# Kernel optimization log

Measured on AMD Instinct MI355X. Metric: run time of the kernel, lower is better.

The kernel has to match this reference:

```python
import jax, jax.numpy as jnp
import numpy as np

N_HEADS = 8
LN_EPS = 1e-5
NEG = -1e9


def _layernorm(x, g, b):
    mu = jnp.mean(x, axis=-1, keepdims=True)
    var = jnp.var(x, axis=-1, keepdims=True)
    return (x - mu) * jax.lax.rsqrt(var + LN_EPS) * g + b


def setup_inputs() -> dict:
    key = jax.random.key(0)
    ks = jax.random.split(key, 16)
    B, T, D, W, L, A = 8, 256, 512, 32, 4, 6
    s = 0.02
    return {
        "feats": jax.random.normal(ks[0], (B, T, D), jnp.float32),
        "pos_embed": jax.random.normal(ks[1], (1, W, D), jnp.float32) * s,
        "Wqkv": jax.random.normal(ks[2], (L, 3 * D, D), jnp.float32) * s,
        "bqkv": jnp.zeros((L, 3 * D), jnp.float32),
        "Wo": jax.random.normal(ks[3], (L, D, D), jnp.float32) * s,
        "bo": jnp.zeros((L, D), jnp.float32),
        "ln1_g": jnp.ones((L, D), jnp.float32),
        "ln1_b": jnp.zeros((L, D), jnp.float32),
        "W1": jax.random.normal(ks[4], (L, 4 * D, D), jnp.float32) * s,
        "b1": jnp.zeros((L, 4 * D), jnp.float32),
        "W2": jax.random.normal(ks[5], (L, D, 4 * D), jnp.float32) * s,
        "b2": jnp.zeros((L, D), jnp.float32),
        "ln2_g": jnp.ones((L, D), jnp.float32),
        "ln2_b": jnp.zeros((L, D), jnp.float32),
        "Wp": jax.random.normal(ks[6], (A, D), jnp.float32) * s,
        "bp": jnp.zeros((A,), jnp.float32),
        "Wv": jax.random.normal(ks[7], (1, D), jnp.float32) * s,
        "bv": jnp.zeros((1,), jnp.float32),
    }


def reference(feats, pos_embed, Wqkv, bqkv, Wo, bo, ln1_g, ln1_b,
              W1, b1, W2, b2, ln2_g, ln2_b, Wp, bp, Wv, bv):
    B, T, D = feats.shape
    W = pos_embed.shape[1]
    L = Wqkv.shape[0]
    H = N_HEADS
    dh = D // H

    # Sliding windows for every timestep t: window slot w holds frame
    # max(t+1-W+w, 0)  (left-pad short prefixes by repeating frame 0).
    idx = jnp.maximum(jnp.arange(T)[:, None] + 1 - W + jnp.arange(W)[None, :], 0)  # (T,W)
    x = feats[:, idx, :].reshape(B * T, W, D) + pos_embed  # (B*T, W, D)

    causal = jnp.tril(jnp.ones((W, W), bool))  # additive -inf upper-tri mask

    for i in range(L):
        qkv = x @ Wqkv[i].T + bqkv[i]                     # (N,W,3D)
        q, k, v = jnp.split(qkv, 3, axis=-1)
        q = q.reshape(-1, W, H, dh).transpose(0, 2, 1, 3)
        k = k.reshape(-1, W, H, dh).transpose(0, 2, 1, 3)
        v = v.reshape(-1, W, H, dh).transpose(0, 2, 1, 3)
        scores = jnp.einsum('nhqd,nhkd->nhqk', q, k) / jnp.sqrt(jnp.float32(dh))
        scores = jnp.where(causal, scores, NEG)
        attn = jax.nn.softmax(scores, axis=-1)
        ctx = jnp.einsum('nhqk,nhkd->nhqd', attn, v)
        ctx = ctx.transpose(0, 2, 1, 3).reshape(-1, W, D)
        x = _layernorm(x + ctx @ Wo[i].T + bo[i], ln1_g[i], ln1_b[i])
        ff = jax.nn.relu(x @ W1[i].T + b1[i]) @ W2[i].T + b2[i]
        x = _layernorm(x + ff, ln2_g[i], ln2_b[i])

    token = x[:, -1, :].reshape(B, T, D)
    logits = token @ Wp.T + bp          # (B,T,A)
    values = (token @ Wv.T + bv)[..., 0]  # (B,T)
    return logits, values
```

## Files before the change

### kernel.cpp

```cpp
#include <hip/hip_runtime.h>
#include <hip/hip_bf16.h>
#include <cstdint>
#include <cstddef>

#define B_    8
#define T_    256
#define D_    512
#define W_    32
#define L_    4
#define A_    6
#define H_    8
#define DH_   64
#define NWIN  (B_*T_)
#define NTOK  (NWIN*W_)
#define FROWS 2176
#define SMALL (NWIN*D_)

typedef __hip_bfloat16 bf16;
using bf16x8 = __attribute__((ext_vector_type(8))) short;
using f32x4  = __attribute__((ext_vector_type(4))) float;
using f32x16 = __attribute__((ext_vector_type(16))) float;

#define XB_BYTES  ((size_t)NTOK * D_ * 2)
#define WQ_ELEMS  ((size_t)L_ * 3*D_*D_)
#define WO_ELEMS  ((size_t)L_ * D_*D_)
#define W1_ELEMS  ((size_t)L_ * 4*D_*D_)
#define W2_ELEMS  ((size_t)L_ * 4*D_*D_)
#define WB_BYTES  ((WQ_ELEMS + WO_ELEMS + W1_ELEMS + W2_ELEMS) * 2)
#define FB_ELEMS  ((size_t)FROWS * D_)
#define QF_ELEMS  ((size_t)FROWS * 3*D_)
#define PPB_ELEMS ((size_t)W_ * 3*D_)
#define SCR_BYTES ((size_t)NTOK * 2560 * 2)
#define TOTAL_BYTES (XB_BYTES + WB_BYTES + (FB_ELEMS + QF_ELEMS)*2 + PPB_ELEMS*4 + SCR_BYTES)

static char* g_fallback = nullptr;
__attribute__((constructor)) static void alloc_fallback() {
    (void)hipMalloc((void**)&g_fallback, TOTAL_BYTES);
}

typedef __attribute__((address_space(3))) uint8_t* as3p;
typedef const __attribute__((address_space(1))) uint8_t* as1p;
__device__ __forceinline__ void gload_lds16(const void* g, void* l) {
    __builtin_amdgcn_global_load_lds((as1p)(const uint8_t*)g,
                                     (as3p)(uint32_t)(uintptr_t)l, 16, 0, 0);
}

__device__ __forceinline__ float bf2f(short s) {
    return __uint_as_float(((uint32_t)(uint16_t)s) << 16);
}
__device__ __forceinline__ short f2bf(float f) {
    return (short)__bfloat16_as_ushort(__float2bfloat16(f));
}

__global__ __launch_bounds__(256) void cvt_kernel(
    const float* __restrict__ w, bf16* __restrict__ o, int n4)
{
    int i = blockIdx.x * 256 + threadIdx.x;
    if (i >= n4) return;
    float4 f = ((const float4*)w)[i];
    bf16* d = o + (size_t)i * 4;
    d[0] = __float2bfloat16(f.x);
    d[1] = __float2bfloat16(f.y);
    d[2] = __float2bfloat16(f.z);
    d[3] = __float2bfloat16(f.w);
}

__global__ __launch_bounds__(256) void build_x_kernel(
    const float* __restrict__ feats,
    const float* __restrict__ pos,
    bf16* __restrict__ xb)
{
    int gid   = blockIdx.x * 256 + threadIdx.x;
    int token = gid >> 7;
    int c4    = (gid & 127) * 4;
    int w     = token & (W_-1);
    int n     = token >> 5;
    int t     = n & (T_-1);
    int b     = n >> 8;
    int frame = t + w - (W_-1); if (frame < 0) frame = 0;
    const float4 f = *(const float4*)(feats + ((size_t)(b*T_ + frame)*D_ + c4));
    const float4 p = *(const float4*)(pos   + ((size_t)w*D_ + c4));
    bf16* d = xb + (size_t)token*D_ + c4;
    d[0] = __float2bfloat16(f.x + p.x);
    d[1] = __float2bfloat16(f.y + p.y);
    d[2] = __float2bfloat16(f.z + p.z);
    d[3] = __float2bfloat16(f.w + p.w);
}

__global__ __launch_bounds__(256) void build_fb_kernel(
    const float* __restrict__ feats,
    const float* __restrict__ pos,
    bf16* __restrict__ fb)
{
    int gid = blockIdx.x * 256 + threadIdx.x;
    int row = gid >> 7;
    int c4  = (gid & 127) * 4;
    bf16* d = fb + (size_t)row * D_ + c4;
    float4 f;
    if (row < 2048)      f = *(const float4*)(feats + (size_t)row * D_ + c4);
    else if (row < 2080) f = *(const float4*)(pos + (size_t)(row - 2048) * D_ + c4);
    else                 f = make_float4(0.f, 0.f, 0.f, 0.f);
    d[0] = __float2bfloat16(f.x);
    d[1] = __float2bfloat16(f.y);
    d[2] = __float2bfloat16(f.z);
    d[3] = __float2bfloat16(f.w);
}

__global__ __launch_bounds__(256) void build_ppb_kernel(
    const bf16* __restrict__ qf,
    const float* __restrict__ bq,
    float* __restrict__ ppb)
{
    int gid = blockIdx.x * 256 + threadIdx.x;
    int w = gid / (3*D_), c = gid % (3*D_);
    ppb[gid] = bf2f(*(const short*)(qf + (size_t)(2048 + w) * (3*D_) + c)) + bq[c];
}

__global__ __launch_bounds__(256) void slice31_kernel(
    const bf16* __restrict__ xb, bf16* __restrict__ xg)
{
    int gid = blockIdx.x * 256 + threadIdx.x;
    int n = gid >> 6, c0 = (gid & 63) * 8;
    *(bf16x8*)(xg + (size_t)n*D_ + c0) =
        *(const bf16x8*)(xb + (size_t)(n*W_ + (W_-1))*D_ + c0);
}

template<bool RELU, bool BIAS, bool REMAP>
__global__ __launch_bounds__(256) void gemm_bf16(
    const bf16* __restrict__ A,
    const bf16* __restrict__ Bt,
    const float* __restrict__ bias,
    bf16* __restrict__ Cb,
    int M, int N, int K)
{
    __shared__ bf16 As[128*32];
    __shared__ bf16 Bs[128*32];

    const int tid  = threadIdx.x;
    const int lane = tid & 63;
    const int wv   = tid >> 6;

    const int gridN = N >> 7;
    const int bid   = blockIdx.x;
    int m0, n0;
    if (REMAP) {
        const int q_ = bid >> 3;
        n0 = (q_ % gridN) << 7;
        m0 = (((q_ / gridN) * 8) + (bid & 7)) << 7;
    } else {
        n0 = (bid % gridN) << 7;
        m0 = (bid / gridN) << 7;
    }

    const int wm = (wv >> 1) * 64;
    const int wn = (wv & 1) * 64;

    f32x16 acc[2][2] = {};

    const int   srow  = wv*16 + (lane >> 2);
    const int   skoff = (lane & 3) * 8;
    const bf16* ga0 = A  + (size_t)(m0 + srow)      * K + skoff;
    const bf16* ga1 = A  + (size_t)(m0 + 64 + srow) * K + skoff;
    const bf16* gb0 = Bt + (size_t)(n0 + srow)      * K + skoff;
    const bf16* gb1 = Bt + (size_t)(n0 + 64 + srow) * K + skoff;
    char* lAs = (char*)As;
    char* lBs = (char*)Bs;
    const int l0 = wv*1024 + lane*16;

    const int r32  = lane & 31;
    const int ksel = (lane >> 5) * 16;

    for (int k0 = 0; k0 < K; k0 += 32) {
        gload_lds16(ga0 + k0, lAs + l0);
        gload_lds16(ga1 + k0, lAs + l0 + 4096);
        gload_lds16(gb0 + k0, lBs + l0);
        gload_lds16(gb1 + k0, lBs + l0 + 4096);
        __syncthreads();

        bf16x8 av[2][2], bv[2][2];
#pragma unroll
        for (int i = 0; i < 2; ++i)
#pragma unroll
            for (int h = 0; h < 2; ++h) {
                av[i][h] = *(const bf16x8*)(lAs + (wm + i*32 + r32)*64 + h*32 + ksel);
                bv[i][h] = *(const bf16x8*)(lBs + (wn + i*32 + r32)*64 + h*32 + ksel);
            }
#pragma unroll
        for (int i = 0; i < 2; ++i)
#pragma unroll
            for (int j = 0; j < 2; ++j) {
                acc[i][j] = __builtin_amdgcn_mfma_f32_32x32x16_bf16(
                    av[i][0], bv[j][0], acc[i][j], 0, 0, 0);
                acc[i][j] = __builtin_amdgcn_mfma_f32_32x32x16_bf16(
                    av[i][1], bv[j][1], acc[i][j], 0, 0, 0);
            }
        __syncthreads();
    }

    const int rbase = (lane >> 5) * 4;
#pragma unroll
    for (int i = 0; i < 2; ++i) {
#pragma unroll
        for (int j = 0; j < 2; ++j) {
            const int ncol = n0 + wn + j*32 + r32;
            const float bv_ = BIAS ? bias[ncol] : 0.f;
#pragma unroll
            for (int reg = 0; reg < 16; ++reg) {
                const int mrow = m0 + wm + i*32 + (reg & 3) + 8*(reg >> 2) + rbase;
                float v = acc[i][j][reg] + bv_;
                if (RELU) v = fmaxf(v, 0.f);
                Cb[(size_t)mrow * N + ncol] = __float2bfloat16(v);
            }
        }
    }
}

template<bool RELU, bool BIAS>
__global__ __launch_bounds__(512, 2) void gemm256(
    const bf16* __restrict__ A,
    const bf16* __restrict__ Bt,
    const float* __restrict__ bias,
    bf16* __restrict__ Cb,
    int M, int N, int K)
{
    (void)M;
    __shared__ bf16 As[2][256*64];
    __shared__ bf16 Bs[2][256*64];

    const int tid  = threadIdx.x;
    const int lane = tid & 63;
    const int wv   = tid >> 6;
    const int wm   = wv >> 2;
    const int wn   = wv & 3;
    const int L    = lane & 15;
    const int qd   = lane >> 4;

    const int gridN = N >> 8;
    const int W8  = gridN << 3;
    const int bid = blockIdx.x;
    const int q_  = bid / W8;
    const int r_  = bid % W8;
    const int n0  = (r_ >> 3) << 8;
    const int m0  = ((q_ << 3) + (r_ & 7)) << 8;

    const int srow = tid >> 3;
    const int scol = ((tid & 7) ^ (srow & 7)) * 8;
    const bf16* gA = A  + (size_t)(m0 + srow) * K + scol;
    const bf16* gB = Bt + (size_t)(n0 + srow) * K + scol;
    const size_t rstep = (size_t)64 * K;
    bf16* lA = &As[0][0] + tid * 8;
    bf16* lB = &Bs[0][0] + tid * 8;

    const int physk0 = ((qd)     ^ (L & 7)) * 8;
    const int physk1 = ((4 + qd) ^ (L & 7)) * 8;
    const int aoff = (wm*128 + L) * 64;
    const int boff = (wn*64  + L) * 64;

    f32x4 acc[8][4] = {};
    bf16x8 av0[4][2], av1[4][2], bv0[2][2], bv1[2][2];

#define STAGE_A2(b, kt) do { \
    const bf16* s_ = gA + (size_t)(kt) * 64; \
    bf16* d_ = lA + (b) * 16384; \
    gload_lds16(s_,            d_); \
    gload_lds16(s_ +   rstep,  d_ + 4096); \
    gload_lds16(s_ + 2*rstep,  d_ + 8192); \
    gload_lds16(s_ + 3*rstep,  d_ + 12288); } while (0)

#define STAGE_B2(b, kt) do { \
    const bf16* s_ = gB + (size_t)(kt) * 64; \
    bf16* d_ = lB + (b) * 16384; \
    gload_lds16(s_,            d_); \
    gload_lds16(s_ +   rstep,  d_ + 4096); \
    gload_lds16(s_ + 2*rstep,  d_ + 8192); \
    gload_lds16(s_ + 3*rstep,  d_ + 12288); } while (0)

#define LDA_(dst, b, qm) do { \
    const bf16* pa_ = &As[b][aoff + (qm)*4096]; \
    _Pragma("unroll") \
    for (int mr_ = 0; mr_ < 4; ++mr_) { \
        dst[mr_][0] = *(const bf16x8*)(pa_ + mr_*1024 + physk0); \
        dst[mr_][1] = *(const bf16x8*)(pa_ + mr_*1024 + physk1); } } while (0)

#define LDB_(dst, b, qn) do { \
    const bf16* pb_ = &Bs[b][boff + (qn)*2048]; \
    _Pragma("unroll") \
    for (int nr_ = 0; nr_ < 2; ++nr_) { \
        dst[nr_][0] = *(const bf16x8*)(pb_ + nr_*1024 + physk0); \
        dst[nr_][1] = *(const bf16x8*)(pb_ + nr_*1024 + physk1); } } while (0)

#define MMA_(qm, qn, av, bv) do { \
    _Pragma("unroll") \
    for (int mr_ = 0; mr_ < 4; ++mr_) \
    _Pragma("unroll") \
    for (int nr_ = 0; nr_ < 2; ++nr_) { \
        f32x4 c_ = acc[(qm)*4+mr_][(qn)*2+nr_]; \
        c_ = __builtin_amdgcn_mfma_f32_16x16x32_bf16(av[mr_][0], bv[nr_][0], c_, 0, 0, 0); \
        c_ = __builtin_amdgcn_mfma_f32_16x16x32_bf16(av[mr_][1], bv[nr_][1], c_, 0, 0, 0); \
        acc[(qm)*4+mr_][(qn)*2+nr_] = c_; } } while (0)

#define BAR_ __builtin_amdgcn_s_barrier()
#define LGKM0_ do { asm volatile("s_waitcnt lgkmcnt(0)" ::: "memory"); \
                    __builtin_amdgcn_sched_barrier(0); } while (0)

#define TILE_(b, kt2) do { \
     \
    LDA_(av0, b, 0); LDB_(bv0, b, 0); \
    BAR_; LGKM0_; \
    __builtin_amdgcn_s_setprio(1); MMA_(0, 0, av0, bv0); __builtin_amdgcn_s_setprio(0); \
    BAR_; \
     \
    LDB_(bv1, b, 1); \
    BAR_; LGKM0_; \
    __builtin_amdgcn_s_setprio(1); MMA_(0, 1, av0, bv1); __builtin_amdgcn_s_setprio(0); \
    BAR_; \
     \
    LDA_(av1, b, 1); \
    STAGE_B2(b, kt2); \
    BAR_; LGKM0_; \
    __builtin_amdgcn_s_setprio(1); MMA_(1, 1, av1, bv1); __builtin_amdgcn_s_setprio(0); \
    BAR_; \
     \
    STAGE_A2(b, kt2); \
    __builtin_amdgcn_s_setprio(1); MMA_(1, 0, av1, bv0); __builtin_amdgcn_s_setprio(0); \
    asm volatile("s_waitcnt vmcnt(8)" ::: "memory"); \
    BAR_; } while (0)

    const int nkt = K >> 6;

    STAGE_B2(0, 0); STAGE_A2(0, 0);
    STAGE_B2(1, 1); STAGE_A2(1, 1);
    asm volatile("s_waitcnt vmcnt(8)" ::: "memory");
    BAR_;

    for (int u = 0; u < nkt; u += 2) {
        int k2 = u + 2; if (k2 >= nkt) k2 -= nkt;
        int k3 = u + 3; if (k3 >= nkt) k3 -= nkt;
        TILE_(0, k2);
        TILE_(1, k3);
    }

    asm volatile("s_waitcnt vmcnt(0)" ::: "memory");

#pragma unroll
    for (int mr = 0; mr < 8; ++mr) {
        const int row = m0 + wm*128 + mr*16 + qd*4;
#pragma unroll
        for (int nr = 0; nr < 4; ++nr) {
            const int col = n0 + wn*64 + nr*16 + L;
            const float bb = BIAS ? bias[col] : 0.f;
            bf16* cp = Cb + (size_t)row * N + col;
#pragma unroll
            for (int rg = 0; rg < 4; ++rg) {
                float v = acc[mr][nr][rg] + bb;
                if (RELU) v = fmaxf(v, 0.f);
                cp[(size_t)rg * N] = __float2bfloat16(v);
            }
        }
    }

#undef STAGE_A2
#undef STAGE_B2
#undef LDA_
#undef LDB_
#undef MMA_
#undef BAR_
#undef LGKM0_
#undef TILE_
}

__global__ __launch_bounds__(256) void lnres_kernel(
    const bf16* __restrict__ y,
    const bf16* __restrict__ xin,
    bf16* __restrict__ xout,
    const float* __restrict__ g,
    const float* __restrict__ b,
    int xin_stride)
{
    const int wave  = threadIdx.x >> 6;
    const int lane  = threadIdx.x & 63;
    const int token = blockIdx.x * 4 + wave;
    const int c0    = lane * 8;

    const bf16* yr = y    + (size_t)token * D_ + c0;
    const bf16* xr = xin  + (size_t)token * xin_stride + c0;
    bf16*       xo = xout + (size_t)token * D_ + c0;

    bf16x8 ty = *(const bf16x8*)yr;
    bf16x8 tx = *(const bf16x8*)xr;

    float v[8];
    float s1 = 0.f, s2 = 0.f;
#pragma unroll
    for (int j = 0; j < 8; ++j) {
        v[j] = bf2f(ty[j]) + bf2f(tx[j]);
        s1 += v[j]; s2 += v[j]*v[j];
    }
#pragma unroll
    for (int mask = 1; mask < 64; mask <<= 1) {
        s1 += __shfl_xor(s1, mask);
        s2 += __shfl_xor(s2, mask);
    }
    const float mu = s1 * (1.f / D_);
    float var = s2 * (1.f / D_) - mu * mu;
    if (var < 0.f) var = 0.f;
    const float rs = rsqrtf(var + 1e-5f);

    const float4 g0 = *(const float4*)(g + c0);
    const float4 g1 = *(const float4*)(g + c0 + 4);
    const float4 b0 = *(const float4*)(b + c0);
    const float4 b1 = *(const float4*)(b + c0 + 4);
    const float gg[8] = {g0.x,g0.y,g0.z,g0.w,g1.x,g1.y,g1.z,g1.w};
    const float bb[8] = {b0.x,b0.y,b0.z,b0.w,b1.x,b1.y,b1.z,b1.w};

    bf16x8 o;
#pragma unroll
    for (int j = 0; j < 8; ++j) {
        float t = (v[j] - mu) * rs * gg[j] + bb[j];
        o[j] = f2bf(t);
    }
    *(bf16x8*)xo = o;
}

__global__ __launch_bounds__(256) void attn_mfma(
    const bf16* __restrict__ qkv,
    bf16* __restrict__ ctx)
{
    __shared__ short Pb[4][32*32];

    const int tid  = threadIdx.x;
    const int lane = tid & 63;
    const int wv   = tid >> 6;
    const int pair = blockIdx.x * 4 + wv;
    const int win  = pair >> 3;
    const int h    = pair & 7;

    const int quad = lane >> 4;
    const int col  = lane & 15;

    const bf16* base = qkv + (size_t)win * W_ * (3*D_) + h * DH_;

    bf16x8 bvv[4];
    {
        const short* vbase = (const short*)(base + 2*D_);
#pragma unroll
        for (int ntd = 0; ntd < 4; ++ntd)
#pragma unroll
            for (int jj = 0; jj < 8; ++jj)
                bvv[ntd][jj] = vbase[(size_t)(quad*8 + jj) * (3*D_) + ntd*16 + col];
    }

    bf16x8 aq[2][2], bk[2][2];
#pragma unroll
    for (int mt = 0; mt < 2; ++mt)
#pragma unroll
        for (int kq = 0; kq < 2; ++kq)
            aq[mt][kq] = *(const bf16x8*)(base + (size_t)(mt*16 + col) * (3*D_)
                                          + kq*32 + quad*8);
#pragma unroll
    for (int nt = 0; nt < 2; ++nt)
#pragma unroll
        for (int kq = 0; kq < 2; ++kq)
            bk[nt][kq] = *(const bf16x8*)(base + D_ + (size_t)(nt*16 + col) * (3*D_)
                                          + kq*32 + quad*8);

    f32x4 S[2][2] = {};
#pragma unroll
    for (int mt = 0; mt < 2; ++mt)
#pragma unroll
        for (int nt = 0; nt < 2; ++nt) {
            S[mt][nt] = __builtin_amdgcn_mfma_f32_16x16x32_bf16(
                aq[mt][0], bk[nt][0], S[mt][nt], 0, 0, 0);
            S[mt][nt] = __builtin_amdgcn_mfma_f32_16x16x32_bf16(
                aq[mt][1], bk[nt][1], S[mt][nt], 0, 0, 0);
        }

    short* P = Pb[wv];
#pragma unroll
    for (int mt = 0; mt < 2; ++mt) {
#pragma unroll
        for (int reg = 0; reg < 4; ++reg) {
            const int row = mt*16 + quad*4 + reg;
            float v0 = (col      <= row) ? S[mt][0][reg] * 0.125f : -1e30f;
            float v1 = (16 + col <= row) ? S[mt][1][reg] * 0.125f : -1e30f;
            float mx = fmaxf(v0, v1);
#pragma unroll
            for (int m = 1; m < 16; m <<= 1) mx = fmaxf(mx, __shfl_xor(mx, m));
            float e0 = __expf(v0 - mx);
            float e1 = __expf(v1 - mx);
            float sm = e0 + e1;
#pragma unroll
            for (int m = 1; m < 16; m <<= 1) sm += __shfl_xor(sm, m);
            float inv = 1.f / sm;
            P[row*32 + col]      = f2bf(e0 * inv);
            P[row*32 + 16 + col] = f2bf(e1 * inv);
        }
    }

    bf16* cb = ctx + (size_t)win * W_ * D_ + h * DH_;
#pragma unroll
    for (int mt = 0; mt < 2; ++mt) {
        bf16x8 ap = *(const bf16x8*)(P + (mt*16 + col)*32 + quad*8);
#pragma unroll
        for (int ntd = 0; ntd < 4; ++ntd) {
            f32x4 O = {};
            O = __builtin_amdgcn_mfma_f32_16x16x32_bf16(ap, bvv[ntd], O, 0, 0, 0);
#pragma unroll
            for (int reg = 0; reg < 4; ++reg) {
                const int row = mt*16 + quad*4 + reg;
                cb[(size_t)row * D_ + ntd*16 + col] = __float2bfloat16(O[reg]);
            }
        }
    }
}

__global__ __launch_bounds__(256) void attn_mfma0(
    const bf16* __restrict__ qf,
    const float* __restrict__ ppb,
    bf16* __restrict__ ctx)
{
    __shared__ short Pb[4][32*32];

    const int tid  = threadIdx.x;
    const int lane = tid & 63;
    const int wv   = tid >> 6;
    const int pair = blockIdx.x * 4 + wv;
    const int win  = pair >> 3;
    const int h    = pair & 7;

    const int quad = lane >> 4;
    const int col  = lane & 15;
    const int bb_  = win >> 8;
    const int tt_  = win & (T_-1);

#define FR_(w) ((size_t)(bb_*T_ + ((tt_ + (w) - (W_-1)) > 0 ? (tt_ + (w) - (W_-1)) : 0)) * (3*D_))

    bf16x8 bvv[4];
#pragma unroll
    for (int ntd = 0; ntd < 4; ++ntd)
#pragma unroll
        for (int jj = 0; jj < 8; ++jj) {
            const int w2 = quad*8 + jj;
            const int c  = 2*D_ + h*DH_ + ntd*16 + col;
            bvv[ntd][jj] = f2bf(bf2f(*(const short*)(qf + FR_(w2) + c))
                                + ppb[w2*(3*D_) + c]);
        }

    bf16x8 aq[2][2], bk[2][2];
#pragma unroll
    for (int mt = 0; mt < 2; ++mt)
#pragma unroll
        for (int kq = 0; kq < 2; ++kq) {
            const int w  = mt*16 + col;
            const size_t fro = FR_(w);
            const int cq = h*DH_ + kq*32 + quad*8;
            const bf16x8 a = *(const bf16x8*)(qf + fro + cq);
            const bf16x8 k = *(const bf16x8*)(qf + fro + D_ + cq);
            const float* pq = ppb + w*(3*D_) + cq;
            const float* pk = pq + D_;
#pragma unroll
            for (int j = 0; j < 8; ++j) {
                aq[mt][kq][j] = f2bf(bf2f(a[j]) + pq[j]);
                bk[mt][kq][j] = f2bf(bf2f(k[j]) + pk[j]);
            }
        }
#undef FR_

    f32x4 S[2][2] = {};
#pragma unroll
    for (int mt = 0; mt < 2; ++mt)
#pragma unroll
        for (int nt = 0; nt < 2; ++nt) {
            S[mt][nt] = __builtin_amdgcn_mfma_f32_16x16x32_bf16(
                aq[mt][0], bk[nt][0], S[mt][nt], 0, 0, 0);
            S[mt][nt] = __builtin_amdgcn_mfma_f32_16x16x32_bf16(
                aq[mt][1], bk[nt][1], S[mt][nt], 0, 0, 0);
        }

    short* P = Pb[wv];
#pragma unroll
    for (int mt = 0; mt < 2; ++mt) {
#pragma unroll
        for (int reg = 0; reg < 4; ++reg) {
            const int row = mt*16 + quad*4 + reg;
            float v0 = (col      <= row) ? S[mt][0][reg] * 0.125f : -1e30f;
            float v1 = (16 + col <= row) ? S[mt][1][reg] * 0.125f : -1e30f;
            float mx = fmaxf(v0, v1);
#pragma unroll
            for (int m = 1; m < 16; m <<= 1) mx = fmaxf(mx, __shfl_xor(mx, m));
            float e0 = __expf(v0 - mx);
            float e1 = __expf(v1 - mx);
            float sm = e0 + e1;
#pragma unroll
            for (int m = 1; m < 16; m <<= 1) sm += __shfl_xor(sm, m);
            float inv = 1.f / sm;
            P[row*32 + col]      = f2bf(e0 * inv);
            P[row*32 + 16 + col] = f2bf(e1 * inv);
        }
    }

    bf16* cb = ctx + (size_t)win * W_ * D_ + h * DH_;
#pragma unroll
    for (int mt = 0; mt < 2; ++mt) {
        bf16x8 ap = *(const bf16x8*)(P + (mt*16 + col)*32 + quad*8);
#pragma unroll
        for (int ntd = 0; ntd < 4; ++ntd) {
            f32x4 O = {};
            O = __builtin_amdgcn_mfma_f32_16x16x32_bf16(ap, bvv[ntd], O, 0, 0, 0);
#pragma unroll
            for (int reg = 0; reg < 4; ++reg) {
                const int row = mt*16 + quad*4 + reg;
                cb[(size_t)row * D_ + ntd*16 + col] = __float2bfloat16(O[reg]);
            }
        }
    }
}

__global__ __launch_bounds__(256) void attn_last2(
    const bf16* __restrict__ kv,
    const bf16* __restrict__ q31,
    bf16* __restrict__ ctxl)
{
    __shared__ float Ps[4][32];

    const int wv   = threadIdx.x >> 6;
    const int lane = threadIdx.x & 63;
    const int pair = blockIdx.x * 4 + wv;
    const int win  = pair >> 3;
    const int h    = pair & 7;

    const bf16* kb   = kv + (size_t)win * W_ * 1024 + h * DH_;
    const short* qrow = (const short*)(q31 + (size_t)win * D_ + h * DH_);

    const int k    = lane & 31;
    const int half = lane >> 5;
    const short* krow = (const short*)(kb + (size_t)k * 1024 + half*32);

    float s = 0.f;
    const bf16x8* q8 = (const bf16x8*)(qrow + half*32);
    const bf16x8* k8 = (const bf16x8*)krow;
#pragma unroll
    for (int c = 0; c < 4; ++c) {
        bf16x8 qa = q8[c], kb_ = k8[c];
#pragma unroll
        for (int j = 0; j < 8; ++j) s += bf2f(qa[j]) * bf2f(kb_[j]);
    }
    s += __shfl_xor(s, 32);
    s *= 0.125f;

    float mx = s;
#pragma unroll
    for (int m = 1; m < 32; m <<= 1) mx = fmaxf(mx, __shfl_xor(mx, m));
    float e = __expf(s - mx);
    float sum = e;
#pragma unroll
    for (int m = 1; m < 32; m <<= 1) sum += __shfl_xor(sum, m);
    if (half == 0) Ps[wv][k] = e / sum;
    __syncthreads();

    const short* vb = (const short*)(kb + 512);
    float o = 0.f;
#pragma unroll
    for (int kk = 0; kk < 32; ++kk)
        o += Ps[wv][kk] * bf2f(vb[(size_t)kk * 1024 + lane]);

    ctxl[(size_t)win * D_ + h * DH_ + lane] = __float2bfloat16(o);
}

__global__ __launch_bounds__(64) void head_kernel(
    const bf16* __restrict__ xq,
    const float* __restrict__ Wp, const float* __restrict__ bp,
    const float* __restrict__ Wv, const float* __restrict__ bv,
    float* __restrict__ out)
{
    const int n    = blockIdx.x;
    const int lane = threadIdx.x;
    const bf16* row = xq + (size_t)n * D_;
    float t[8];
#pragma unroll
    for (int j = 0; j < 8; ++j) t[j] = bf2f(*(const short*)(row + lane + j*64));

    for (int a = 0; a < A_ + 1; ++a) {
        const float* w = (a < A_) ? (Wp + (size_t)a * D_) : Wv;
        float d = 0.f;
#pragma unroll
        for (int j = 0; j < 8; ++j) d += t[j] * w[lane + j*64];
#pragma unroll
        for (int off = 32; off > 0; off >>= 1) d += __shfl_down(d, off);
        if (lane == 0) {
            if (a < A_) out[(size_t)n*A_ + a] = d + bp[a];
            else        out[(size_t)NWIN*A_ + n] = d + bv[0];
        }
    }
}

extern "C" void kernel_launch(void* const* d_in, const int* in_sizes, int n_in,
                              void* d_out, int out_size, void* d_ws, size_t ws_size,
                              hipStream_t stream) {
    const float* feats = (const float*)d_in[0];
    const float* pos   = (const float*)d_in[1];
    const float* Wqkv  = (const float*)d_in[2];
    const float* bqkv  = (const float*)d_in[3];
    const float* Wo    = (const float*)d_in[4];
    const float* bo    = (const float*)d_in[5];
    const float* ln1g  = (const float*)d_in[6];
    const float* ln1b  = (const float*)d_in[7];
    const float* W1    = (const float*)d_in[8];
    const float* b1    = (const float*)d_in[9];
    const float* W2    = (const float*)d_in[10];
    const float* b2    = (const float*)d_in[11];
    const float* ln2g  = (const float*)d_in[12];
    const float* ln2b  = (const float*)d_in[13];
    const float* Wp    = (const float*)d_in[14];
    const float* bp    = (const float*)d_in[15];
    const float* Wv    = (const float*)d_in[16];
    const float* bv    = (const float*)d_in[17];
    float* out = (float*)d_out;

    char* basep = (ws_size >= TOTAL_BYTES) ? (char*)d_ws : g_fallback;

    bf16*  xb   = (bf16*)basep;
    bf16*  wq_b = (bf16*)(basep + XB_BYTES);
    bf16*  wo_b = wq_b + WQ_ELEMS;
    bf16*  w1_b = wo_b + WO_ELEMS;
    bf16*  w2_b = w1_b + W1_ELEMS;
    bf16*  fb   = w2_b + W2_ELEMS;
    bf16*  qf   = fb + FB_ELEMS;
    float* ppb  = (float*)(qf + QF_ELEMS);
    bf16*  scr  = (bf16*)(ppb + PPB_ELEMS);
    bf16*  qkv_s = scr;
    bf16*  kv_s  = scr;
    bf16*  ctx_s = scr + (size_t)NTOK * (3*D_);
    bf16*  h_s   = scr;
    bf16*  y_s   = scr + (size_t)NTOK * 2048;
    bf16*  ctxl = ctx_s;
    bf16*  ysm  = ctx_s + (size_t)SMALL;
    bf16*  hsm  = ctx_s + (size_t)2*SMALL;
    bf16*  xq   = ctx_s + (size_t)6*SMALL;
    bf16*  xg   = ctx_s + (size_t)8*SMALL;
    bf16*  q31  = ctx_s + (size_t)9*SMALL;

    cvt_kernel<<<(WQ_ELEMS/4 + 255)/256, 256, 0, stream>>>(Wqkv, wq_b, WQ_ELEMS/4);
    cvt_kernel<<<(WO_ELEMS/4 + 255)/256, 256, 0, stream>>>(Wo,   wo_b, WO_ELEMS/4);
    cvt_kernel<<<(W1_ELEMS/4 + 255)/256, 256, 0, stream>>>(W1,   w1_b, W1_ELEMS/4);
    cvt_kernel<<<(W2_ELEMS/4 + 255)/256, 256, 0, stream>>>(W2,   w2_b, W2_ELEMS/4);

    build_x_kernel<<<NTOK * (D_/4) / 256, 256, 0, stream>>>(feats, pos, xb);
    build_fb_kernel<<<FROWS * (D_/4) / 256, 256, 0, stream>>>(feats, pos, fb);

    const int GM2 = NTOK / 256;

    for (int i = 0; i < L_; ++i) {
        const bf16*  wq_i = wq_b + (size_t)i * 3*D_*D_;
        const float* bq_i = bqkv + (size_t)i * 3*D_;
        const bf16*  wo_i = wo_b + (size_t)i * D_*D_;
        const float* bo_i = bo   + (size_t)i * D_;
        const bf16*  w1_i = w1_b + (size_t)i * 4*D_*D_;
        const float* b1_i = b1   + (size_t)i * 4*D_;
        const bf16*  w2_i = w2_b + (size_t)i * 4*D_*D_;
        const float* b2_i = b2   + (size_t)i * D_;

        if (i == 0) {
            gemm_bf16<false,false,false><<<(FROWS/128) * (3*D_/128), 256, 0, stream>>>(
                fb, wq_i, nullptr, qf, FROWS, 3*D_, D_);
            build_ppb_kernel<<<W_*(3*D_)/256, 256, 0, stream>>>(qf, bq_i, ppb);
            attn_mfma0<<<NWIN * H_ / 4, 256, 0, stream>>>(qf, ppb, ctx_s);
        } else if (i < L_-1) {
            gemm256<false,true><<<GM2 * (3*D_/256), 512, 0, stream>>>(
                xb, wq_i, bq_i, qkv_s, NTOK, 3*D_, D_);
            attn_mfma<<<NWIN * H_ / 4, 256, 0, stream>>>(qkv_s, ctx_s);
        }

        if (i < L_-1) {
            gemm256<false,true><<<GM2 * (D_/256), 512, 0, stream>>>(
                ctx_s, wo_i, bo_i, y_s, NTOK, D_, D_);
            lnres_kernel<<<NTOK/4, 256, 0, stream>>>(
                y_s, xb, xb, ln1g + (size_t)i*D_, ln1b + (size_t)i*D_, D_);
            gemm256<true,true><<<GM2 * (4*D_/256), 512, 0, stream>>>(
                xb, w1_i, b1_i, h_s, NTOK, 4*D_, D_);
            gemm256<false,true><<<GM2 * (D_/256), 512, 0, stream>>>(
                h_s, w2_i, b2_i, y_s, NTOK, D_, 4*D_);
            lnres_kernel<<<NTOK/4, 256, 0, stream>>>(
                y_s, xb, xb, ln2g + (size_t)i*D_, ln2b + (size_t)i*D_, D_);
        } else {
            gemm256<false,true><<<GM2 * (1024/256), 512, 0, stream>>>(
                xb, wq_i + (size_t)D_*D_, bq_i + D_, kv_s, NTOK, 2*D_, D_);
            slice31_kernel<<<NWIN*64/256, 256, 0, stream>>>(xb, xg);
            gemm_bf16<false,true,false><<<(NWIN/128) * (D_/128), 256, 0, stream>>>(
                xg, wq_i, bq_i, q31, NWIN, D_, D_);
            attn_last2<<<NWIN * H_ / 4, 256, 0, stream>>>(kv_s, q31, ctxl);
            gemm_bf16<false,true,false><<<(NWIN/128) * (D_/128), 256, 0, stream>>>(
                ctxl, wo_i, bo_i, ysm, NWIN, D_, D_);
            lnres_kernel<<<NWIN/4, 256, 0, stream>>>(
                ysm, xg, xq,
                ln1g + (size_t)i*D_, ln1b + (size_t)i*D_, D_);
            gemm_bf16<true,true,false><<<(NWIN/128) * (4*D_/128), 256, 0, stream>>>(
                xq, w1_i, b1_i, hsm, NWIN, 4*D_, D_);
            gemm_bf16<false,true,false><<<(NWIN/128) * (D_/128), 256, 0, stream>>>(
                hsm, w2_i, b2_i, ysm, NWIN, D_, 4*D_);
            lnres_kernel<<<NWIN/4, 256, 0, stream>>>(
                ysm, xq, xq, ln2g + (size_t)i*D_, ln2b + (size_t)i*D_, D_);
        }
    }

    head_kernel<<<NWIN, 64, 0, stream>>>(xq, Wp, bp, Wv, bv, out);
}
```

Baseline: 2.056 ms.

## Fuse Wo and W2 GEMMs with residual add and LayerNorm

Measured after the change: 2.236 ms. 1.09x slower.

```diff
diff --git a/kernel.cpp b/kernel.cpp
--- a/kernel.cpp
+++ b/kernel.cpp
@@ -369,6 +369,157 @@
 #undef TILE_
 }
 
+__global__ __launch_bounds__(512, 2) void gemmln(
+    const bf16* __restrict__ A,
+    const bf16* __restrict__ Bt,
+    const float* __restrict__ bias,
+    bf16* __restrict__ xb,
+    const float* __restrict__ g,
+    const float* __restrict__ b,
+    int K)
+{
+    __shared__ bf16 As[3*128*32];
+    __shared__ bf16 Bs[3*512*32];
+
+    const int tid  = threadIdx.x;
+    const int lane = tid & 63;
+    const int wv   = tid >> 6;
+    const int wm   = wv >> 2;
+    const int wn   = wv & 3;
+    const int L    = lane & 15;
+    const int qd   = lane >> 4;
+
+    const int m0 = blockIdx.x << 7;
+
+    const int srow = tid >> 2;
+    const int slog = (tid & 3) ^ ((srow >> 1) & 3);
+    const bf16* gA = A  + (size_t)(m0 + srow) * K + slog * 8;
+    const bf16* gB = Bt + (size_t)srow * K + slog * 8;
+    const size_t rb = (size_t)128 * K;
+    bf16* lA = As + tid * 8;
+    bf16* lB = Bs + tid * 8;
+
+    const int kch  = (qd ^ ((L >> 1) & 3)) * 8;
+    const int aoff = (wm*64  + L) * 32 + kch;
+    const int boff = (wn*128 + L) * 32 + kch;
+
+    f32x4 acc[4][8] = {};
+
+#define STG_(buf, kt) do { \
+    gload_lds16(gA + (size_t)(kt) * 32, lA + (buf) * 4096); \
+    const bf16* s_ = gB + (size_t)(kt) * 32; \
+    bf16* d_ = lB + (buf) * 16384; \
+    gload_lds16(s_,         d_); \
+    gload_lds16(s_ +   rb,  d_ + 4096); \
+    gload_lds16(s_ + 2*rb,  d_ + 8192); \
+    gload_lds16(s_ + 3*rb,  d_ + 12288); } while (0)
+
+#define BAR_ __builtin_amdgcn_s_barrier()
+
+    const int nt = K >> 5;
+
+    STG_(0, 0);
+    STG_(1, 1);
+    asm volatile("s_waitcnt vmcnt(5)" ::: "memory");
+    BAR_;
+
+    int b0 = 0;
+    for (int t = 0; t < nt; ++t) {
+        const int tgt = (b0 + 2 >= 3) ? b0 - 1 : b0 + 2;
+        const int kt2 = (t + 2 < nt) ? t + 2 : t;
+        STG_(tgt, kt2);
+
+        bf16x8 av[4], bv[8];
+        const bf16* pa = As + b0*4096  + aoff;
+        const bf16* pb = Bs + b0*16384 + boff;
+#pragma unroll
+        for (int mr = 0; mr < 4; ++mr) av[mr] = *(const bf16x8*)(pa + mr*512);
+#pragma unroll
+        for (int nr = 0; nr < 8; ++nr) bv[nr] = *(const bf16x8*)(pb + nr*512);
+        asm volatile("s_waitcnt lgkmcnt(0)" ::: "memory");
+        __builtin_amdgcn_sched_barrier(0);
+        __builtin_amdgcn_s_setprio(1);
+#pragma unroll
+        for (int mr = 0; mr < 4; ++mr)
+#pragma unroll
+            for (int nr = 0; nr < 8; ++nr)
+                acc[mr][nr] = __builtin_amdgcn_mfma_f32_16x16x32_bf16(
+                    av[mr], bv[nr], acc[mr][nr], 0, 0, 0);
+        __builtin_amdgcn_s_setprio(0);
+        asm volatile("s_waitcnt vmcnt(5)" ::: "memory");
+        BAR_;
+        b0 = (b0 == 2) ? 0 : b0 + 1;
+    }
+
+    asm volatile("s_waitcnt vmcnt(0)" ::: "memory");
+    BAR_;
+
+    float* lnred = (float*)As;
+
+    float bias8[8], gg8[8], bb8[8];
+#pragma unroll
+    for (int nr = 0; nr < 8; ++nr) {
+        const int col = wn*128 + nr*16 + L;
+        bias8[nr] = bias[col];
+        gg8[nr]   = g[col];
+        bb8[nr]   = b[col];
+    }
+
+#pragma unroll
+    for (int mr = 0; mr < 4; ++mr) {
+#pragma unroll
+        for (int rg = 0; rg < 4; ++rg) {
+            const int row = wm*64 + mr*16 + qd*4 + rg;
+            const bf16* xr = xb + (size_t)(m0 + row) * D_ + wn*128 + L;
+            float ps = 0.f, pq = 0.f;
+#pragma unroll
+            for (int nr = 0; nr < 8; ++nr) {
+                float s = acc[mr][nr][rg] + bias8[nr]
+                        + bf2f(*(const short*)(xr + nr*16));
+                acc[mr][nr][rg] = s;
+                ps += s; pq += s*s;
+            }
+#pragma unroll
+            for (int m = 1; m < 16; m <<= 1) {
+                ps += __shfl_xor(ps, m);
+                pq += __shfl_xor(pq, m);
+            }
+            if (L == 0) {
+                lnred[(wn*128 + row)*2    ] = ps;
+                lnred[(wn*128 + row)*2 + 1] = pq;
+            }
+        }
+    }
+    BAR_;
+
+#pragma unroll
+    for (int mr = 0; mr < 4; ++mr) {
+#pragma unroll
+        for (int rg = 0; rg < 4; ++rg) {
+            const int row = wm*64 + mr*16 + qd*4 + rg;
+            float S = 0.f, Q = 0.f;
+#pragma unroll
+            for (int w4 = 0; w4 < 4; ++w4) {
+                S += lnred[(w4*128 + row)*2    ];
+                Q += lnred[(w4*128 + row)*2 + 1];
+            }
+            const float mu = S * (1.f / D_);
+            float var = Q * (1.f / D_) - mu * mu;
+            if (var < 0.f) var = 0.f;
+            const float rs = rsqrtf(var + 1e-5f);
+            bf16* xw = xb + (size_t)(m0 + row) * D_ + wn*128 + L;
+#pragma unroll
+            for (int nr = 0; nr < 8; ++nr) {
+                float o = (acc[mr][nr][rg] - mu) * rs * gg8[nr] + bb8[nr];
+                *(short*)(xw + nr*16) = f2bf(o);
+            }
+        }
+    }
+
+#undef STG_
+#undef BAR_
+}
+
 __global__ __launch_bounds__(256) void lnres_kernel(
     const bf16* __restrict__ y,
     const bf16* __restrict__ xin,
@@ -732,7 +883,6 @@
     bf16*  kv_s  = scr;
     bf16*  ctx_s = scr + (size_t)NTOK * (3*D_);
     bf16*  h_s   = scr;
-    bf16*  y_s   = scr + (size_t)NTOK * 2048;
     bf16*  ctxl = ctx_s;
     bf16*  ysm  = ctx_s + (size_t)SMALL;
     bf16*  hsm  = ctx_s + (size_t)2*SMALL;
@@ -749,6 +899,7 @@
     build_fb_kernel<<<FROWS * (D_/4) / 256, 256, 0, stream>>>(feats, pos, fb);
 
     const int GM2 = NTOK / 256;
+    const int GL  = NTOK / 128;
 
     for (int i = 0; i < L_; ++i) {
         const bf16*  wq_i = wq_b + (size_t)i * 3*D_*D_;
@@ -772,16 +923,14 @@
         }
 
         if (i < L_-1) {
-            gemm256<false,true><<<GM2 * (D_/256), 512, 0, stream>>>(
-                ctx_s, wo_i, bo_i, y_s, NTOK, D_, D_);
-            lnres_kernel<<<NTOK/4, 256, 0, stream>>>(
-                y_s, xb, xb, ln1g + (size_t)i*D_, ln1b + (size_t)i*D_, D_);
+            gemmln<<<GL, 512, 0, stream>>>(
+                ctx_s, wo_i, bo_i, xb,
+                ln1g + (size_t)i*D_, ln1b + (size_t)i*D_, D_);
             gemm256<true,true><<<GM2 * (4*D_/256), 512, 0, stream>>>(
                 xb, w1_i, b1_i, h_s, NTOK, 4*D_, D_);
-            gemm256<false,true><<<GM2 * (D_/256), 512, 0, stream>>>(
-                h_s, w2_i, b2_i, y_s, NTOK, D_, 4*D_);
-            lnres_kernel<<<NTOK/4, 256, 0, stream>>>(
-                y_s, xb, xb, ln2g + (size_t)i*D_, ln2b + (size_t)i*D_, D_);
+            gemmln<<<GL, 512, 0, stream>>>(
+                h_s, w2_i, b2_i, xb,
+                ln2g + (size_t)i*D_, ln2b + (size_t)i*D_, 4*D_);
         } else {
             gemm256<false,true><<<GM2 * (1024/256), 512, 0, stream>>>(
                 xb, wq_i + (size_t)D_*D_, bq_i + D_, kv_s, NTOK, 2*D_, D_);
```

## Use persistent multi-panel GEMM kernel for FFN layers with fixed grid

Applied to the files above, without the earlier changes.

Result: faster. 1.999 ms (-2.8%).

```diff
diff --git a/kernel.cpp b/kernel.cpp
--- a/kernel.cpp
+++ b/kernel.cpp
@@ -369,6 +369,165 @@
 #undef TILE_
 }
 
+template<bool RELU, int LOG2NKT, int NPAN>
+__global__ __launch_bounds__(512, 2) void gemm256m(
+    const bf16* __restrict__ A,
+    const bf16* __restrict__ Bt,
+    const float* __restrict__ bias,
+    bf16* __restrict__ Cb,
+    int N)
+{
+    constexpr int NKT = 1 << LOG2NKT;
+    constexpr int K   = NKT * 64;
+    constexpr int NT  = NPAN * NKT;
+
+    __shared__ bf16 As[2][256*64];
+    __shared__ bf16 Bs[2][256*64];
+
+    const int tid  = threadIdx.x;
+    const int lane = tid & 63;
+    const int wv   = tid >> 6;
+    const int wm   = wv >> 2;
+    const int wn   = wv & 3;
+    const int L    = lane & 15;
+    const int qd   = lane >> 4;
+
+    const int gridN = N >> 8;
+    const int SETS  = 256 / gridN;
+    const int bid   = blockIdx.x;
+    const int sI    = bid % SETS;
+    const int n0    = (bid / SETS) << 8;
+
+    const int srow = tid >> 3;
+    const int scol = ((tid & 7) ^ (srow & 7)) * 8;
+    const bf16* gA0 = A  + (size_t)srow * K + scol;
+    const bf16* gB  = Bt + (size_t)(n0 + srow) * K + scol;
+    const size_t rstep = (size_t)64 * K;
+    bf16* lA = &As[0][0] + tid * 8;
+    bf16* lB = &Bs[0][0] + tid * 8;
+
+    const int physk0 = ((qd)     ^ (L & 7)) * 8;
+    const int physk1 = ((4 + qd) ^ (L & 7)) * 8;
+    const int aoff = (wm*128 + L) * 64;
+    const int boff = (wn*64  + L) * 64;
+
+    f32x4 acc[8][4] = {};
+    bf16x8 av0[4][2], av1[4][2], bv0[2][2], bv1[2][2];
+
+#define MSTAGE_A(b, tau) do { \
+    const int p2_ = (tau) >> LOG2NKT, k2_ = (tau) & (NKT-1); \
+    const bf16* s_ = gA0 + ((size_t)(sI + SETS*p2_) << 8) * K + (size_t)k2_ * 64; \
+    bf16* d_ = lA + (b) * 16384; \
+    gload_lds16(s_,            d_); \
+    gload_lds16(s_ +   rstep,  d_ + 4096); \
+    gload_lds16(s_ + 2*rstep,  d_ + 8192); \
+    gload_lds16(s_ + 3*rstep,  d_ + 12288); } while (0)
+
+#define MSTAGE_B(b, tau) do { \
+    const bf16* s_ = gB + (size_t)((tau) & (NKT-1)) * 64; \
+    bf16* d_ = lB + (b) * 16384; \
+    gload_lds16(s_,            d_); \
+    gload_lds16(s_ +   rstep,  d_ + 4096); \
+    gload_lds16(s_ + 2*rstep,  d_ + 8192); \
+    gload_lds16(s_ + 3*rstep,  d_ + 12288); } while (0)
+
+#define MLDA(dst, b, qm) do { \
+    const bf16* pa_ = &As[b][aoff + (qm)*4096]; \
+    _Pragma("unroll") \
+    for (int mr_ = 0; mr_ < 4; ++mr_) { \
+        dst[mr_][0] = *(const bf16x8*)(pa_ + mr_*1024 + physk0); \
+        dst[mr_][1] = *(const bf16x8*)(pa_ + mr_*1024 + physk1); } } while (0)
+
+#define MLDB(dst, b, qn) do { \
+    const bf16* pb_ = &Bs[b][boff + (qn)*2048]; \
+    _Pragma("unroll") \
+    for (int nr_ = 0; nr_ < 2; ++nr_) { \
+        dst[nr_][0] = *(const bf16x8*)(pb_ + nr_*1024 + physk0); \
+        dst[nr_][1] = *(const bf16x8*)(pb_ + nr_*1024 + physk1); } } while (0)
+
+#define MMMA(qm, qn, av, bv) do { \
+    _Pragma("unroll") \
+    for (int mr_ = 0; mr_ < 4; ++mr_) \
+    _Pragma("unroll") \
+    for (int nr_ = 0; nr_ < 2; ++nr_) { \
+        f32x4 c_ = acc[(qm)*4+mr_][(qn)*2+nr_]; \
+        c_ = __builtin_amdgcn_mfma_f32_16x16x32_bf16(av[mr_][0], bv[nr_][0], c_, 0, 0, 0); \
+        c_ = __builtin_amdgcn_mfma_f32_16x16x32_bf16(av[mr_][1], bv[nr_][1], c_, 0, 0, 0); \
+        acc[(qm)*4+mr_][(qn)*2+nr_] = c_; } } while (0)
+
+#define MBAR __builtin_amdgcn_s_barrier()
+#define MLGKM0 do { asm volatile("s_waitcnt lgkmcnt(0)" ::: "memory"); \
+                    __builtin_amdgcn_sched_barrier(0); } while (0)
+
+#define MTILE(b, tau2) do { \
+     \
+    MLDA(av0, b, 0); MLDB(bv0, b, 0); \
+    MBAR; MLGKM0; \
+    __builtin_amdgcn_s_setprio(1); MMMA(0, 0, av0, bv0); __builtin_amdgcn_s_setprio(0); \
+    MBAR; \
+     \
+    MLDB(bv1, b, 1); \
+    MBAR; MLGKM0; \
+    __builtin_amdgcn_s_setprio(1); MMMA(0, 1, av0, bv1); __builtin_amdgcn_s_setprio(0); \
+    MBAR; \
+     \
+    MLDA(av1, b, 1); \
+    MSTAGE_B(b, tau2); \
+    MBAR; MLGKM0; \
+    __builtin_amdgcn_s_setprio(1); MMMA(1, 1, av1, bv1); __builtin_amdgcn_s_setprio(0); \
+    MBAR; \
+     \
+    MSTAGE_A(b, tau2); \
+    __builtin_amdgcn_s_setprio(1); MMMA(1, 0, av1, bv0); __builtin_amdgcn_s_setprio(0); \
+    asm volatile("s_waitcnt vmcnt(8)" ::: "memory"); \
+    MBAR; } while (0)
+
+    MSTAGE_B(0, 0); MSTAGE_A(0, 0);
+    MSTAGE_B(1, 1); MSTAGE_A(1, 1);
+    asm volatile("s_waitcnt vmcnt(8)" ::: "memory");
+    MBAR;
+
+    for (int u = 0; u < NT; u += 2) {
+        const int t2 = (u + 2 < NT) ? u + 2 : u;
+        const int t3 = (u + 3 < NT) ? u + 3 : u + 1;
+        MTILE(0, t2);
+        MTILE(1, t3);
+
+        if (((u + 1) & (NKT - 1)) == NKT - 1) {
+            const int panel = (u + 1) >> LOG2NKT;
+            const int mbase = (sI + SETS * panel) << 8;
+#pragma unroll
+            for (int mr = 0; mr < 8; ++mr) {
+                const int row = mbase + wm*128 + mr*16 + qd*4;
+#pragma unroll
+                for (int nr = 0; nr < 4; ++nr) {
+                    const int col = n0 + wn*64 + nr*16 + L;
+                    const float bb = bias[col];
+                    bf16* cp = Cb + (size_t)row * N + col;
+#pragma unroll
+                    for (int rg = 0; rg < 4; ++rg) {
+                        float v = acc[mr][nr][rg] + bb;
+                        if (RELU) v = fmaxf(v, 0.f);
+                        cp[(size_t)rg * N] = __float2bfloat16(v);
+                    }
+                    acc[mr][nr] = (f32x4){0.f, 0.f, 0.f, 0.f};
+                }
+            }
+        }
+    }
+
+    asm volatile("s_waitcnt vmcnt(0)" ::: "memory");
+
+#undef MSTAGE_A
+#undef MSTAGE_B
+#undef MLDA
+#undef MLDB
+#undef MMMA
+#undef MBAR
+#undef MLGKM0
+#undef MTILE
+}
+
 __global__ __launch_bounds__(256) void lnres_kernel(
     const bf16* __restrict__ y,
     const bf16* __restrict__ xin,
@@ -776,10 +935,10 @@
                 ctx_s, wo_i, bo_i, y_s, NTOK, D_, D_);
             lnres_kernel<<<NTOK/4, 256, 0, stream>>>(
                 y_s, xb, xb, ln1g + (size_t)i*D_, ln1b + (size_t)i*D_, D_);
-            gemm256<true,true><<<GM2 * (4*D_/256), 512, 0, stream>>>(
-                xb, w1_i, b1_i, h_s, NTOK, 4*D_, D_);
-            gemm256<false,true><<<GM2 * (D_/256), 512, 0, stream>>>(
-                h_s, w2_i, b2_i, y_s, NTOK, D_, 4*D_);
+            gemm256m<true,3,8><<<256, 512, 0, stream>>>(
+                xb, w1_i, b1_i, h_s, 4*D_);
+            gemm256m<false,5,2><<<256, 512, 0, stream>>>(
+                h_s, w2_i, b2_i, y_s, D_);
             lnres_kernel<<<NTOK/4, 256, 0, stream>>>(
                 y_s, xb, xb, ln2g + (size_t)i*D_, ln2b + (size_t)i*D_, D_);
         } else {
```

## Make gemm256 persistent with fixed 256-block grid over multiple M panels

Applied to the files above, without the earlier changes.

Result: faster. 1.949 ms (median of 2 runs) (-5.2%).

```diff
diff --git a/kernel.cpp b/kernel.cpp
--- a/kernel.cpp
+++ b/kernel.cpp
@@ -215,15 +215,18 @@
     }
 }
 
-template<bool RELU, bool BIAS>
-__global__ __launch_bounds__(512, 2) void gemm256(
+template<bool RELU, int LOG2NKT, int NPAN>
+__global__ __launch_bounds__(512, 2) void gemm256m(
     const bf16* __restrict__ A,
     const bf16* __restrict__ Bt,
     const float* __restrict__ bias,
     bf16* __restrict__ Cb,
-    int M, int N, int K)
-{
-    (void)M;
+    int N, int ldC)
+{
+    constexpr int NKT = 1 << LOG2NKT;
+    constexpr int K   = NKT * 64;
+    constexpr int NT  = NPAN * NKT;
+
     __shared__ bf16 As[2][256*64];
     __shared__ bf16 Bs[2][256*64];
 
@@ -236,17 +239,15 @@
     const int qd   = lane >> 4;
 
     const int gridN = N >> 8;
-    const int W8  = gridN << 3;
-    const int bid = blockIdx.x;
-    const int q_  = bid / W8;
-    const int r_  = bid % W8;
-    const int n0  = (r_ >> 3) << 8;
-    const int m0  = ((q_ << 3) + (r_ & 7)) << 8;
+    const int SETS  = 256 / gridN;
+    const int bid   = blockIdx.x;
+    const int sI    = bid % SETS;
+    const int n0    = (bid / SETS) << 8;
 
     const int srow = tid >> 3;
     const int scol = ((tid & 7) ^ (srow & 7)) * 8;
-    const bf16* gA = A  + (size_t)(m0 + srow) * K + scol;
-    const bf16* gB = Bt + (size_t)(n0 + srow) * K + scol;
+    const bf16* gA0 = A  + (size_t)srow * K + scol;
+    const bf16* gB  = Bt + (size_t)(n0 + srow) * K + scol;
     const size_t rstep = (size_t)64 * K;
     bf16* lA = &As[0][0] + tid * 8;
     bf16* lB = &Bs[0][0] + tid * 8;
@@ -259,37 +260,38 @@
     f32x4 acc[8][4] = {};
     bf16x8 av0[4][2], av1[4][2], bv0[2][2], bv1[2][2];
 
-#define STAGE_A2(b, kt) do { \
-    const bf16* s_ = gA + (size_t)(kt) * 64; \
+#define MSTAGE_A(b, tau) do { \
+    const int p2_ = (tau) >> LOG2NKT, k2_ = (tau) & (NKT-1); \
+    const bf16* s_ = gA0 + ((size_t)(sI + SETS*p2_) << 8) * K + (size_t)k2_ * 64; \
     bf16* d_ = lA + (b) * 16384; \
     gload_lds16(s_,            d_); \
     gload_lds16(s_ +   rstep,  d_ + 4096); \
     gload_lds16(s_ + 2*rstep,  d_ + 8192); \
     gload_lds16(s_ + 3*rstep,  d_ + 12288); } while (0)
 
-#define STAGE_B2(b, kt) do { \
-    const bf16* s_ = gB + (size_t)(kt) * 64; \
+#define MSTAGE_B(b, tau) do { \
+    const bf16* s_ = gB + (size_t)((tau) & (NKT-1)) * 64; \
     bf16* d_ = lB + (b) * 16384; \
     gload_lds16(s_,            d_); \
     gload_lds16(s_ +   rstep,  d_ + 4096); \
     gload_lds16(s_ + 2*rstep,  d_ + 8192); \
     gload_lds16(s_ + 3*rstep,  d_ + 12288); } while (0)
 
-#define LDA_(dst, b, qm) do { \
+#define MLDA(dst, b, qm) do { \
     const bf16* pa_ = &As[b][aoff + (qm)*4096]; \
     _Pragma("unroll") \
     for (int mr_ = 0; mr_ < 4; ++mr_) { \
         dst[mr_][0] = *(const bf16x8*)(pa_ + mr_*1024 + physk0); \
         dst[mr_][1] = *(const bf16x8*)(pa_ + mr_*1024 + physk1); } } while (0)
 
-#define LDB_(dst, b, qn) do { \
+#define MLDB(dst, b, qn) do { \
     const bf16* pb_ = &Bs[b][boff + (qn)*2048]; \
     _Pragma("unroll") \
     for (int nr_ = 0; nr_ < 2; ++nr_) { \
         dst[nr_][0] = *(const bf16x8*)(pb_ + nr_*1024 + physk0); \
         dst[nr_][1] = *(const bf16x8*)(pb_ + nr_*1024 + physk1); } } while (0)
 
-#define MMA_(qm, qn, av, bv) do { \
+#define MMMA(qm, qn, av, bv) do { \
     _Pragma("unroll") \
     for (int mr_ = 0; mr_ < 4; ++mr_) \
     _Pragma("unroll") \
@@ -299,74 +301,77 @@
         c_ = __builtin_amdgcn_mfma_f32_16x16x32_bf16(av[mr_][1], bv[nr_][1], c_, 0, 0, 0); \
         acc[(qm)*4+mr_][(qn)*2+nr_] = c_; } } while (0)
 
-#define BAR_ __builtin_amdgcn_s_barrier()
-#define LGKM0_ do { asm volatile("s_waitcnt lgkmcnt(0)" ::: "memory"); \
+#define MBAR __builtin_amdgcn_s_barrier()
+#define MLGKM0 do { asm volatile("s_waitcnt lgkmcnt(0)" ::: "memory"); \
                     __builtin_amdgcn_sched_barrier(0); } while (0)
 
-#define TILE_(b, kt2) do { \
+#define MTILE(b, tau2) do { \
      \
-    LDA_(av0, b, 0); LDB_(bv0, b, 0); \
-    BAR_; LGKM0_; \
-    __builtin_amdgcn_s_setprio(1); MMA_(0, 0, av0, bv0); __builtin_amdgcn_s_setprio(0); \
-    BAR_; \
+    MLDA(av0, b, 0); MLDB(bv0, b, 0); \
+    MBAR; MLGKM0; \
+    __builtin_amdgcn_s_setprio(1); MMMA(0, 0, av0, bv0); __builtin_amdgcn_s_setprio(0); \
+    MBAR; \
      \
-    LDB_(bv1, b, 1); \
-    BAR_; LGKM0_; \
-    __builtin_amdgcn_s_setprio(1); MMA_(0, 1, av0, bv1); __builtin_amdgcn_s_setprio(0); \
-    BAR_; \
+    MLDB(bv1, b, 1); \
+    MBAR; MLGKM0; \
+    __builtin_amdgcn_s_setprio(1); MMMA(0, 1, av0, bv1); __builtin_amdgcn_s_setprio(0); \
+    MBAR; \
      \
-    LDA_(av1, b, 1); \
-    STAGE_B2(b, kt2); \
-    BAR_; LGKM0_; \
-    __builtin_amdgcn_s_setprio(1); MMA_(1, 1, av1, bv1); __builtin_amdgcn_s_setprio(0); \
-    BAR_; \
+    MLDA(av1, b, 1); \
+    MSTAGE_B(b, tau2); \
+    MBAR; MLGKM0; \
+    __builtin_amdgcn_s_setprio(1); MMMA(1, 1, av1, bv1); __builtin_amdgcn_s_setprio(0); \
+    MBAR; \
      \
-    STAGE_A2(b, kt2); \
-    __builtin_amdgcn_s_setprio(1); MMA_(1, 0, av1, bv0); __builtin_amdgcn_s_setprio(0); \
+    MSTAGE_A(b, tau2); \
+    __builtin_amdgcn_s_setprio(1); MMMA(1, 0, av1, bv0); __builtin_amdgcn_s_setprio(0); \
     asm volatile("s_waitcnt vmcnt(8)" ::: "memory"); \
-    BAR_; } while (0)
-
-    const int nkt = K >> 6;
-
-    STAGE_B2(0, 0); STAGE_A2(0, 0);
-    STAGE_B2(1, 1); STAGE_A2(1, 1);
+    MBAR; } while (0)
+
+    MSTAGE_B(0, 0); MSTAGE_A(0, 0);
+    MSTAGE_B(1, 1); MSTAGE_A(1, 1);
     asm volatile("s_waitcnt vmcnt(8)" ::: "memory");
-    BAR_;
-
-    for (int u = 0; u < nkt; u += 2) {
-        int k2 = u + 2; if (k2 >= nkt) k2 -= nkt;
-        int k3 = u + 3; if (k3 >= nkt) k3 -= nkt;
-        TILE_(0, k2);
-        TILE_(1, k3);
+    MBAR;
+
+    for (int u = 0; u < NT; u += 2) {
+        const int t2 = (u + 2 < NT) ? u + 2 : u;
+        const int t3 = (u + 3 < NT) ? u + 3 : u + 1;
+        MTILE(0, t2);
+        MTILE(1, t3);
+
+        if (((u + 1) & (NKT - 1)) == NKT - 1) {
+            const int panel = (u + 1) >> LOG2NKT;
+            const int mbase = (sI + SETS * panel) << 8;
+#pragma unroll
+            for (int mr = 0; mr < 8; ++mr) {
+                const int row = mbase + wm*128 + mr*16 + qd*4;
+#pragma unroll
+                for (int nr = 0; nr < 4; ++nr) {
+                    const int col = n0 + wn*64 + nr*16 + L;
+                    const float bb = bias[col];
+                    bf16* cp = Cb + (size_t)row * ldC + col;
+#pragma unroll
+                    for (int rg = 0; rg < 4; ++rg) {
+                        float v = acc[mr][nr][rg] + bb;
+                        if (RELU) v = fmaxf(v, 0.f);
+                        cp[(size_t)rg * ldC] = __float2bfloat16(v);
+                    }
+                    acc[mr][nr] = (f32x4){0.f, 0.f, 0.f, 0.f};
+                }
+            }
+        }
     }
 
     asm volatile("s_waitcnt vmcnt(0)" ::: "memory");
 
-#pragma unroll
-    for (int mr = 0; mr < 8; ++mr) {
-        const int row = m0 + wm*128 + mr*16 + qd*4;
-#pragma unroll
-        for (int nr = 0; nr < 4; ++nr) {
-            const int col = n0 + wn*64 + nr*16 + L;
-            const float bb = BIAS ? bias[col] : 0.f;
-            bf16* cp = Cb + (size_t)row * N + col;
-#pragma unroll
-            for (int rg = 0; rg < 4; ++rg) {
-                float v = acc[mr][nr][rg] + bb;
-                if (RELU) v = fmaxf(v, 0.f);
-                cp[(size_t)rg * N] = __float2bfloat16(v);
-            }
-        }
-    }
-
-#undef STAGE_A2
-#undef STAGE_B2
-#undef LDA_
-#undef LDB_
-#undef MMA_
-#undef BAR_
-#undef LGKM0_
-#undef TILE_
+#undef MSTAGE_A
+#undef MSTAGE_B
+#undef MLDA
+#undef MLDB
+#undef MMMA
+#undef MBAR
+#undef MLGKM0
+#undef MTILE
 }
 
 __global__ __launch_bounds__(256) void lnres_kernel(
@@ -748,8 +753,6 @@
     build_x_kernel<<<NTOK * (D_/4) / 256, 256, 0, stream>>>(feats, pos, xb);
     build_fb_kernel<<<FROWS * (D_/4) / 256, 256, 0, stream>>>(feats, pos, fb);
 
-    const int GM2 = NTOK / 256;
-
     for (int i = 0; i < L_; ++i) {
         const bf16*  wq_i = wq_b + (size_t)i * 3*D_*D_;
         const float* bq_i = bqkv + (size_t)i * 3*D_;
@@ -766,25 +769,27 @@
             build_ppb_kernel<<<W_*(3*D_)/256, 256, 0, stream>>>(qf, bq_i, ppb);
             attn_mfma0<<<NWIN * H_ / 4, 256, 0, stream>>>(qf, ppb, ctx_s);
         } else if (i < L_-1) {
-            gemm256<false,true><<<GM2 * (3*D_/256), 512, 0, stream>>>(
-                xb, wq_i, bq_i, qkv_s, NTOK, 3*D_, D_);
+            gemm256m<false,3,2><<<256, 512, 0, stream>>>(
+                xb, wq_i, bq_i, qkv_s, 512, 3*D_);
+            gemm256m<false,3,4><<<256, 512, 0, stream>>>(
+                xb, wq_i + (size_t)D_*D_, bq_i + D_, qkv_s + D_, 1024, 3*D_);
             attn_mfma<<<NWIN * H_ / 4, 256, 0, stream>>>(qkv_s, ctx_s);
         }
 
         if (i < L_-1) {
-            gemm256<false,true><<<GM2 * (D_/256), 512, 0, stream>>>(
-                ctx_s, wo_i, bo_i, y_s, NTOK, D_, D_);
+            gemm256m<false,3,2><<<256, 512, 0, stream>>>(
+                ctx_s, wo_i, bo_i, y_s, D_, D_);
             lnres_kernel<<<NTOK/4, 256, 0, stream>>>(
                 y_s, xb, xb, ln1g + (size_t)i*D_, ln1b + (size_t)i*D_, D_);
-            gemm256<true,true><<<GM2 * (4*D_/256), 512, 0, stream>>>(
-                xb, w1_i, b1_i, h_s, NTOK, 4*D_, D_);
-            gemm256<false,true><<<GM2 * (D_/256), 512, 0, stream>>>(
-                h_s, w2_i, b2_i, y_s, NTOK, D_, 4*D_);
+            gemm256m<true,3,8><<<256, 512, 0, stream>>>(
+                xb, w1_i, b1_i, h_s, 4*D_, 4*D_);
+            gemm256m<false,5,2><<<256, 512, 0, stream>>>(
+                h_s, w2_i, b2_i, y_s, D_, D_);
             lnres_kernel<<<NTOK/4, 256, 0, stream>>>(
                 y_s, xb, xb, ln2g + (size_t)i*D_, ln2b + (size_t)i*D_, D_);
         } else {
-            gemm256<false,true><<<GM2 * (1024/256), 512, 0, stream>>>(
-                xb, wq_i + (size_t)D_*D_, bq_i + D_, kv_s, NTOK, 2*D_, D_);
+            gemm256m<false,3,4><<<256, 512, 0, stream>>>(
+                xb, wq_i + (size_t)D_*D_, bq_i + D_, kv_s, 1024, 1024);
             slice31_kernel<<<NWIN*64/256, 256, 0, stream>>>(xb, xg);
             gemm_bf16<false,true,false><<<(NWIN/128) * (D_/128), 256, 0, stream>>>(
                 xg, wq_i, bq_i, q31, NWIN, D_, D_);
```
